# Kernel tuning notes

Measured on AMD Instinct MI355X. Metric: run time of the kernel, lower is better.

## Reference

```python
import jax, jax.numpy as jnp
import numpy as np

SPATIAL_SHAPES = [(128, 128), (64, 64), (32, 32), (16, 16)]  # (H_l, W_l) per level
NUM_HEADS = 8
NUM_LEVELS = 4
NUM_POINTS = 4
EMBED_DIM = 256
HEAD_DIM = EMBED_DIM // NUM_HEADS
LEN_V = sum(h * w for h, w in SPATIAL_SHAPES)  # 21760
BS, LQ = 8, 900


def setup_inputs() -> dict:
    key = jax.random.key(0)
    ks = jax.random.split(key, 12)
    s = 0.05
    return {
        'query': jax.random.normal(ks[0], (BS, LQ, EMBED_DIM), jnp.float32),
        'reference_points': jax.random.uniform(ks[1], (BS, LQ, NUM_LEVELS, 2), jnp.float32),
        'value': jax.random.normal(ks[2], (BS, LEN_V, EMBED_DIM), jnp.float32),
        'w_value': jax.random.normal(ks[3], (EMBED_DIM, EMBED_DIM), jnp.float32) * s,
        'b_value': jnp.zeros((EMBED_DIM,), jnp.float32),
        'w_off': jax.random.normal(ks[4], (EMBED_DIM, NUM_HEADS * NUM_LEVELS * NUM_POINTS * 2), jnp.float32) * s,
        'b_off': jax.random.normal(ks[5], (NUM_HEADS * NUM_LEVELS * NUM_POINTS * 2,), jnp.float32),
        'w_attn': jax.random.normal(ks[6], (EMBED_DIM, NUM_HEADS * NUM_LEVELS * NUM_POINTS), jnp.float32) * s,
        'b_attn': jnp.zeros((NUM_HEADS * NUM_LEVELS * NUM_POINTS,), jnp.float32),
        'w_out': jax.random.normal(ks[7], (EMBED_DIM, EMBED_DIM), jnp.float32) * s,
        'b_out': jnp.zeros((EMBED_DIM,), jnp.float32),
    }


def _bilinear_sample(val, locx, locy, H, W):
    # val: [bs, nh, H*W, hd]; locx/locy: [bs, nh, N] normalized in [0,1]
    # grid_sample semantics: align_corners=False, zero padding.
    px = locx * W - 0.5
    py = locy * H - 0.5
    x0 = jnp.floor(px)
    y0 = jnp.floor(py)
    dx = px - x0
    dy = py - y0
    x0i = x0.astype(jnp.int32)
    y0i = y0.astype(jnp.int32)
    out = jnp.zeros(val.shape[:2] + (locx.shape[-1], val.shape[-1]), val.dtype)
    corners = [
        (x0i, y0i, (1 - dx) * (1 - dy)),
        (x0i + 1, y0i, dx * (1 - dy)),
        (x0i, y0i + 1, (1 - dx) * dy),
        (x0i + 1, y0i + 1, dx * dy),
    ]
    for xi, yi, w in corners:
        valid = ((xi >= 0) & (xi < W) & (yi >= 0) & (yi < H)).astype(val.dtype)
        idx = jnp.clip(yi, 0, H - 1) * W + jnp.clip(xi, 0, W - 1)
        g = jnp.take_along_axis(val, idx[..., None], axis=2)  # [bs,nh,N,hd]
        out = out + g * (w * valid)[..., None]
    return out


def reference(query, reference_points, value, w_value, b_value, w_off, b_off,
              w_attn, b_attn, w_out, b_out):
    bs, Lq, C = query.shape
    # value projection -> [bs, Lv, nh, hd]
    v = (value @ w_value + b_value).reshape(bs, -1, NUM_HEADS, HEAD_DIM)
    # sampling offsets [bs,Lq,nh,L,P,2], attention weights softmax over L*P
    off = (query @ w_off + b_off).reshape(bs, Lq, NUM_HEADS, NUM_LEVELS, NUM_POINTS, 2)
    aw = (query @ w_attn + b_attn).reshape(bs, Lq, NUM_HEADS, NUM_LEVELS * NUM_POINTS)
    aw = jax.nn.softmax(aw, axis=-1).reshape(bs, Lq, NUM_HEADS, NUM_LEVELS, NUM_POINTS)
    # normalizer is (W_l, H_l) per level (flip of spatial shapes)
    norm = jnp.asarray([[w, h] for h, w in SPATIAL_SHAPES], query.dtype)  # [L,2]
    loc = reference_points[:, :, None, :, None, :] + off / norm[None, None, None, :, None, :]
    # per-level bilinear sampling and weighted reduction
    out = jnp.zeros((bs, Lq, NUM_HEADS, HEAD_DIM), query.dtype)
    start = 0
    for l, (H, W) in enumerate(SPATIAL_SHAPES):
        vl = v[:, start:start + H * W]                       # [bs,HW,nh,hd]
        vl = vl.transpose(0, 2, 1, 3)                        # [bs,nh,HW,hd]
        ll = loc[:, :, :, l].transpose(0, 2, 1, 3, 4)        # [bs,nh,Lq,P,2]
        ll = ll.reshape(bs, NUM_HEADS, Lq * NUM_POINTS, 2)
        s = _bilinear_sample(vl, ll[..., 0], ll[..., 1], H, W)
        s = s.reshape(bs, NUM_HEADS, Lq, NUM_POINTS, HEAD_DIM)
        out = out + jnp.einsum('bhqpd,bqhp->bqhd', s, aw[:, :, :, l])
        start += H * W
    out = out.reshape(bs, Lq, C)
    return out @ w_out + b_out
```

## Files before the change

kernel.cpp:

```cpp
#include <hip/hip_runtime.h>

#define BS 8
#define LQ 900
#define NH 8
#define NL 4
#define NP 4
#define HD 32
#define ED 256
#define LEN_V 21760

typedef __attribute__((ext_vector_type(8))) short bf16x8;
typedef __attribute__((ext_vector_type(4))) float f32x4;
typedef __attribute__((ext_vector_type(4))) float fv4;

static __device__ __forceinline__ unsigned short f2bf(float f) {
  union { float f; unsigned u; } x; x.f = f;
  unsigned r = x.u + 0x7fffu + ((x.u >> 16) & 1u);
  return (unsigned short)(r >> 16);
}
static __device__ __forceinline__ float bf_lo(unsigned u) {
  union { unsigned u; float f; } x; x.u = u << 16;
  return x.f;
}
static __device__ __forceinline__ float bf_hi(unsigned u) {
  union { unsigned u; float f; } x; x.u = u & 0xffff0000u;
  return x.f;
}
static __device__ __forceinline__ unsigned pack2(float a, float b) {
  return (unsigned)f2bf(a) | ((unsigned)f2bf(b) << 16);
}

__global__ __launch_bounds__(256) void bprep_kernel(
    const float* __restrict__ w, unsigned short* __restrict__ Bsw) {
  const int id = blockIdx.x * 256 + threadIdx.x;
  const int n = id & 255;
  const int kseg = (id >> 8) & 3;
  const int kc = id >> 10;
  const float* src = &w[(kc * 32 + kseg * 8) * 256 + n];
  float f[8];
#pragma unroll
  for (int j = 0; j < 8; j++) f[j] = src[j * 256];
  uint4 pk;
  pk.x = pack2(f[0], f[1]);
  pk.y = pack2(f[2], f[3]);
  pk.z = pack2(f[4], f[5]);
  pk.w = pack2(f[6], f[7]);
  *(uint4*)&Bsw[((kc * 4 + kseg) * 256 + n) * 8] = pk;
}

__global__ __launch_bounds__(256, 4) void vproj_kernel(
    const float* __restrict__ value, const unsigned short* __restrict__ Bsw,
    const float* __restrict__ bias, unsigned short* __restrict__ vout) {
  const int t = threadIdx.x;
  const int row0 = blockIdx.x * 64;
  const int wv = t >> 6;
  const int lane = t & 63;
  const int quad = lane >> 4;
  const int nn = lane & 15;

  __shared__ unsigned short a_lds[4 * 64 * 8];

  f32x4 acc[4][4];
#pragma unroll
  for (int i = 0; i < 4; i++)
#pragma unroll
    for (int j = 0; j < 4; j++) acc[i][j] = (f32x4)(0.f);

  const int arow = t >> 2;
  const int akseg = t & 3;
  const unsigned short* bptr = &Bsw[(quad * 256 + wv * 64 + nn) * 8];

  for (int kc = 0; kc < 8; kc++) {
    __syncthreads();
    {
      const float* pa = &value[(row0 + arow) * 256 + kc * 32 + akseg * 8];
      fv4 v0 = __builtin_nontemporal_load((const fv4*)pa);
      fv4 v1 = __builtin_nontemporal_load((const fv4*)(pa + 4));
      uint4 pk;
      pk.x = pack2(v0.x, v0.y);
      pk.y = pack2(v0.z, v0.w);
      pk.z = pack2(v1.x, v1.y);
      pk.w = pack2(v1.z, v1.w);
      *(uint4*)&a_lds[(akseg * 64 + arow) * 8] = pk;
    }
    __syncthreads();

    bf16x8 af[4], bfr[4];
#pragma unroll
    for (int ct = 0; ct < 4; ct++)
      bfr[ct] = *(const bf16x8*)(bptr + (kc * 1024 + ct * 16) * 8);
#pragma unroll
    for (int rt = 0; rt < 4; rt++)
      af[rt] = *(const bf16x8*)&a_lds[(quad * 64 + rt * 16 + nn) * 8];
#pragma unroll
    for (int rt = 0; rt < 4; rt++)
#pragma unroll
      for (int ct = 0; ct < 4; ct++)
        acc[rt][ct] = __builtin_amdgcn_mfma_f32_16x16x32_bf16(
            af[rt], bfr[ct], acc[rt][ct], 0, 0, 0);
  }

  const int bb = row0 / LEN_V;
  const int s0 = row0 - bb * LEN_V;
#pragma unroll
  for (int ct = 0; ct < 4; ct++) {
    const int col = wv * 64 + ct * 16 + nn;
    const float bv = bias[col];
    const int h = col >> 5;
    const int d = col & 31;
    unsigned short* vb = &vout[((bb * NH + h) * LEN_V + s0) * HD + d];
#pragma unroll
    for (int rt = 0; rt < 4; rt++) {
      f32x4 f = acc[rt][ct];
#pragma unroll
      for (int reg = 0; reg < 4; reg++) {
        const int s = rt * 16 + quad * 4 + reg;
        vb[s * HD] = f2bf(f[reg] + bv);
      }
    }
  }
}

__global__ __launch_bounds__(384, 2) void offattn_kernel(
    const float* __restrict__ query,
    const float* __restrict__ w_off, const float* __restrict__ b_off,
    const float* __restrict__ w_attn, const float* __restrict__ b_attn,
    float* __restrict__ OFF, float* __restrict__ LOG) {
  const int t = threadIdx.x;
  const int row0 = blockIdx.x * 32;
  const int rg = t / 96;
  const int c4 = t % 96;
  const int col = c4 * 4;
  const bool isOff = col < 256;
  const float* wbase = isOff ? (w_off + col) : (w_attn + (col - 256));
  const int wstride = isOff ? 256 : 128;
  const float* bb = isOff ? (b_off + col) : (b_attn + (col - 256));
  __shared__ float a_lds[32][8];

  float4 acc[8];
#pragma unroll
  for (int r = 0; r < 8; r++) acc[r] = make_float4(0.f, 0.f, 0.f, 0.f);

  for (int k0 = 0; k0 < 256; k0 += 8) {
    __syncthreads();
    if (t < 256) a_lds[t >> 3][t & 7] = query[(row0 + (t >> 3)) * 256 + k0 + (t & 7)];
    __syncthreads();
    float4 wr[8];
#pragma unroll
    for (int k = 0; k < 8; k++)
      wr[k] = *(const float4*)&wbase[(k0 + k) * wstride];
#pragma unroll
    for (int r = 0; r < 8; r++) {
      const float* ar = &a_lds[rg * 8 + r][0];
      float4 a0 = *(const float4*)&ar[0];
      float4 a1 = *(const float4*)&ar[4];
      float4 s = acc[r];
      s.x += a0.x*wr[0].x + a0.y*wr[1].x + a0.z*wr[2].x + a0.w*wr[3].x
           + a1.x*wr[4].x + a1.y*wr[5].x + a1.z*wr[6].x + a1.w*wr[7].x;
      s.y += a0.x*wr[0].y + a0.y*wr[1].y + a0.z*wr[2].y + a0.w*wr[3].y
           + a1.x*wr[4].y + a1.y*wr[5].y + a1.z*wr[6].y + a1.w*wr[7].y;
      s.z += a0.x*wr[0].z + a0.y*wr[1].z + a0.z*wr[2].z + a0.w*wr[3].z
           + a1.x*wr[4].z + a1.y*wr[5].z + a1.z*wr[6].z + a1.w*wr[7].z;
      s.w += a0.x*wr[0].w + a0.y*wr[1].w + a0.z*wr[2].w + a0.w*wr[3].w
           + a1.x*wr[4].w + a1.y*wr[5].w + a1.z*wr[6].w + a1.w*wr[7].w;
      acc[r] = s;
    }
  }

  const float4 bv = *(const float4*)bb;
#pragma unroll
  for (int r = 0; r < 8; r++) {
    const int grow = row0 + rg * 8 + r;
    float4 o = make_float4(acc[r].x + bv.x, acc[r].y + bv.y,
                           acc[r].z + bv.z, acc[r].w + bv.w);
    if (isOff) *(float4*)&OFF[grow * 256 + col] = o;
    else       *(float4*)&LOG[grow * 128 + (col - 256)] = o;
  }
}

__global__ __launch_bounds__(256, 6) void sample_kernel(
    const float* __restrict__ refp, const unsigned short* __restrict__ vp,
    const float* __restrict__ OFF, const float* __restrict__ LOG,
    float* __restrict__ RES) {
  const int t = threadIdx.x;
  const int b = blockIdx.x / (LQ / 4);
  const int q0 = (blockIdx.x % (LQ / 4)) * 4;

  __shared__ float off_lds[4][256];
  __shared__ float aw_lds[4][128];
  __shared__ float ref_lds[4][4][2];
  __shared__ int   soff[512][4];
  __shared__ float swt[512][4];

#pragma unroll
  for (int qi = 0; qi < 4; qi++)
    off_lds[qi][t] = OFF[(b * LQ + q0 + qi) * 256 + t];
  if (t < 128) {
#pragma unroll
    for (int qi = 0; qi < 4; qi++)
      aw_lds[qi][t] = LOG[(b * LQ + q0 + qi) * 128 + t];
  }
  if (t < 32) {
    const int qi = t >> 3, l = (t >> 1) & 3, xy = t & 1;
    ref_lds[qi][l][xy] = refp[((b * LQ + q0 + qi) * NL + l) * 2 + xy];
  }
  __syncthreads();

  if (t < 32) {
    const int qi = t >> 3, h = t & 7;
    float* a = &aw_lds[qi][h * 16];
    float m = a[0];
#pragma unroll
    for (int i = 1; i < 16; i++) m = fmaxf(m, a[i]);
    float e[16];
    float ssum = 0.f;
#pragma unroll
    for (int i = 0; i < 16; i++) { e[i] = __expf(a[i] - m); ssum += e[i]; }
    const float inv = 1.f / ssum;
#pragma unroll
    for (int i = 0; i < 16; i++) a[i] = e[i] * inv;
  }
  __syncthreads();

#pragma unroll
  for (int ss = 0; ss < 2; ss++) {
    const int sid = t + ss * 256;
    const int p = sid & 3, l = (sid >> 2) & 3, h = (sid >> 4) & 7, qi = sid >> 7;
    const int W = 128 >> l;
    const int base = (l == 0) ? 0 : ((l == 1) ? 16384 : ((l == 2) ? 20480 : 21504));
    const float Wf = (float)W;
    const float refx = ref_lds[qi][l][0];
    const float refy = ref_lds[qi][l][1];
    const float offx = off_lds[qi][h * 32 + l * 8 + p * 2 + 0];
    const float offy = off_lds[qi][h * 32 + l * 8 + p * 2 + 1];
    const float aw = aw_lds[qi][h * 16 + l * 4 + p];
    const float px = refx * Wf + offx - 0.5f;
    const float py = refy * Wf + offy - 0.5f;
    const float x0f = floorf(px), y0f = floorf(py);
    const float dx = px - x0f, dy = py - y0f;
    const int x0 = (int)x0f, y0 = (int)y0f;
    const int x1 = x0 + 1, y1 = y0 + 1;
    const float mx0 = (x0 >= 0 && x0 < W) ? 1.f : 0.f;
    const float mx1 = (x1 >= 0 && x1 < W) ? 1.f : 0.f;
    const float my0 = (y0 >= 0 && y0 < W) ? 1.f : 0.f;
    const float my1 = (y1 >= 0 && y1 < W) ? 1.f : 0.f;
    const int x0c = min(max(x0, 0), W - 1);
    const int x1c = min(max(x1, 0), W - 1);
    const int y0c = min(max(y0, 0), W - 1);
    const int y1c = min(max(y1, 0), W - 1);
    soff[sid][0] = (base + y0c * W + x0c) * 8;
    soff[sid][1] = (base + y0c * W + x1c) * 8;
    soff[sid][2] = (base + y1c * W + x0c) * 8;
    soff[sid][3] = (base + y1c * W + x1c) * 8;
    swt[sid][0] = (1.f - dx) * (1.f - dy) * mx0 * my0 * aw;
    swt[sid][1] = dx * (1.f - dy) * mx1 * my0 * aw;
    swt[sid][2] = (1.f - dx) * dy * mx0 * my1 * aw;
    swt[sid][3] = dx * dy * mx1 * my1 * aw;
  }
  __syncthreads();

  const int qi = t >> 6;
  const int hh = (t >> 3) & 7;
  const int d4 = t & 7;
  const uint2* vpu2 = (const uint2*)vp + (size_t)(b * NH + hh) * (LEN_V * HD / 4);
  float r0 = 0.f, r1 = 0.f, r2 = 0.f, r3 = 0.f;
  const int sbase = (qi * 8 + hh) << 4;
#pragma unroll 4
  for (int lp = 0; lp < 16; lp++) {
    const int sid = sbase + lp;
    const int4 o = *(const int4*)&soff[sid][0];
    const float4 w = *(const float4*)&swt[sid][0];
    const uint2 u00 = vpu2[o.x + d4];
    const uint2 u10 = vpu2[o.y + d4];
    const uint2 u01 = vpu2[o.z + d4];
    const uint2 u11 = vpu2[o.w + d4];
    r0 += w.x * bf_lo(u00.x) + w.y * bf_lo(u10.x) + w.z * bf_lo(u01.x) + w.w * bf_lo(u11.x);
    r1 += w.x * bf_hi(u00.x) + w.y * bf_hi(u10.x) + w.z * bf_hi(u01.x) + w.w * bf_hi(u11.x);
    r2 += w.x * bf_lo(u00.y) + w.y * bf_lo(u10.y) + w.z * bf_lo(u01.y) + w.w * bf_lo(u11.y);
    r3 += w.x * bf_hi(u00.y) + w.y * bf_hi(u10.y) + w.z * bf_hi(u01.y) + w.w * bf_hi(u11.y);
  }
  float4 rr = make_float4(r0, r1, r2, r3);
  *(float4*)&RES[(b * LQ + q0 + qi) * 256 + hh * 32 + d4 * 4] = rr;
}

__global__ __launch_bounds__(256, 2) void outproj_kernel(
    const float* __restrict__ RES, const float* __restrict__ w,
    const float* __restrict__ bias, float* __restrict__ out) {
  const int t = threadIdx.x;
  const int row0 = blockIdx.x * 32;
  const int rg = t >> 6;
  const int c0 = (t & 63) << 2;
  __shared__ float a_lds[32][8];

  float4 acc[8];
#pragma unroll
  for (int r = 0; r < 8; r++) acc[r] = make_float4(0.f, 0.f, 0.f, 0.f);

  const int lr = t >> 3;
  const int lk = t & 7;
  for (int k0 = 0; k0 < 256; k0 += 8) {
    __syncthreads();
    a_lds[lr][lk] = RES[(row0 + lr) * 256 + k0 + lk];
    __syncthreads();
    float4 wr[8];
#pragma unroll
    for (int k = 0; k < 8; k++)
      wr[k] = *(const float4*)&w[(k0 + k) * 256 + c0];
#pragma unroll
    for (int r = 0; r < 8; r++) {
      const float* ar = &a_lds[rg * 8 + r][0];
      float4 a0 = *(const float4*)&ar[0];
      float4 a1 = *(const float4*)&ar[4];
      float4 s = acc[r];
      s.x += a0.x*wr[0].x + a0.y*wr[1].x + a0.z*wr[2].x + a0.w*wr[3].x
           + a1.x*wr[4].x + a1.y*wr[5].x + a1.z*wr[6].x + a1.w*wr[7].x;
      s.y += a0.x*wr[0].y + a0.y*wr[1].y + a0.z*wr[2].y + a0.w*wr[3].y
           + a1.x*wr[4].y + a1.y*wr[5].y + a1.z*wr[6].y + a1.w*wr[7].y;
      s.z += a0.x*wr[0].z + a0.y*wr[1].z + a0.z*wr[2].z + a0.w*wr[3].z
           + a1.x*wr[4].z + a1.y*wr[5].z + a1.z*wr[6].z + a1.w*wr[7].z;
      s.w += a0.x*wr[0].w + a0.y*wr[1].w + a0.z*wr[2].w + a0.w*wr[3].w
           + a1.x*wr[4].w + a1.y*wr[5].w + a1.z*wr[6].w + a1.w*wr[7].w;
      acc[r] = s;
    }
  }

  const float4 bv = *(const float4*)&bias[c0];
#pragma unroll
  for (int r = 0; r < 8; r++) {
    const int grow = row0 + rg * 8 + r;
    float4 o = make_float4(acc[r].x + bv.x, acc[r].y + bv.y,
                           acc[r].z + bv.z, acc[r].w + bv.w);
    *(float4*)&out[grow * 256 + c0] = o;
  }
}

extern "C" void kernel_launch(void* const* d_in, const int* in_sizes, int n_in,
                              void* d_out, int out_size, void* d_ws, size_t ws_size,
                              hipStream_t stream) {
  (void)in_sizes; (void)n_in; (void)out_size; (void)ws_size;
  const float* query   = (const float*)d_in[0];
  const float* refp    = (const float*)d_in[1];
  const float* value   = (const float*)d_in[2];
  const float* w_value = (const float*)d_in[3];
  const float* b_value = (const float*)d_in[4];
  const float* w_off   = (const float*)d_in[5];
  const float* b_off   = (const float*)d_in[6];
  const float* w_attn  = (const float*)d_in[7];
  const float* b_attn  = (const float*)d_in[8];
  const float* w_out   = (const float*)d_in[9];
  const float* b_out   = (const float*)d_in[10];
  float* out = (float*)d_out;

  char* ws = (char*)d_ws;
  unsigned short* vp = (unsigned short*)ws;
  float* OFF = (float*)(ws + 89128960);
  float* LOG = (float*)(ws + 89128960 + 7372800);
  float* RES = (float*)(ws + 89128960 + 7372800 + 3686400);
  unsigned short* Bsw = (unsigned short*)(ws + 89128960 + 7372800 + 3686400 + 7372800);

  bprep_kernel<<<32, 256, 0, stream>>>(w_value, Bsw);
  vproj_kernel<<<(BS * LEN_V) / 64, 256, 0, stream>>>(value, Bsw, b_value, vp);
  offattn_kernel<<<(BS * LQ) / 32, 384, 0, stream>>>(query, w_off, b_off,
                                                     w_attn, b_attn, OFF, LOG);
  sample_kernel<<<BS * (LQ / 4), 256, 0, stream>>>(refp, vp, OFF, LOG, RES);
  outproj_kernel<<<(BS * LQ) / 32, 256, 0, stream>>>(RES, w_out, b_out, out);
}
```

Measured before the change: 423.1 us.

## Restructure sampling blocks per (batch, head) with query chunks and XCD-aware mapping

The sample kernel now assigns each block one (batch, head) pair and a chunk of 32 queries, instead of 4 queries across all heads. The block index is remapped so that consecutive work items from the same (batch, head) land on the same XCD (blockIdx & 7 striping). The goal is to improve L2 locality of the head-specific value plane during the bilinear gathers. In exchange, the last chunk has padding work (900 is not a multiple of 32, so the last chunk is partly wasted), and loads of OFF and LOG rows become narrower strided reads.

```diff
diff --git a/kernel.cpp b/kernel.cpp
--- a/kernel.cpp
+++ b/kernel.cpp
@@ -8,6 +8,9 @@
 #define HD 32
 #define ED 256
 #define LEN_V 21760
+
+#define QB 32
+#define QCHUNKS 29
 
 typedef __attribute__((ext_vector_type(8))) short bf16x8;
 typedef __attribute__((ext_vector_type(4))) float f32x4;
@@ -183,32 +186,40 @@
     const float* __restrict__ OFF, const float* __restrict__ LOG,
     float* __restrict__ RES) {
   const int t = threadIdx.x;
-  const int b = blockIdx.x / (LQ / 4);
-  const int q0 = (blockIdx.x % (LQ / 4)) * 4;
-
-  __shared__ float off_lds[4][256];
-  __shared__ float aw_lds[4][128];
-  __shared__ float ref_lds[4][4][2];
-  __shared__ int   soff[512][4];
-  __shared__ float swt[512][4];
-
-#pragma unroll
-  for (int qi = 0; qi < 4; qi++)
-    off_lds[qi][t] = OFF[(b * LQ + q0 + qi) * 256 + t];
-  if (t < 128) {
-#pragma unroll
-    for (int qi = 0; qi < 4; qi++)
-      aw_lds[qi][t] = LOG[(b * LQ + q0 + qi) * 128 + t];
-  }
-  if (t < 32) {
-    const int qi = t >> 3, l = (t >> 1) & 3, xy = t & 1;
-    ref_lds[qi][l][xy] = refp[((b * LQ + q0 + qi) * NL + l) * 2 + xy];
+  const int work = (blockIdx.x & 7) * (8 * QCHUNKS) + (blockIdx.x >> 3);
+  const int pair = work / QCHUNKS;
+  const int qc   = work - pair * QCHUNKS;
+  const int b = pair >> 3;
+  const int h = pair & 7;
+  const int q0 = qc * QB;
+
+  __shared__ float off_lds[QB][32];
+  __shared__ float aw_lds[QB][16];
+  __shared__ float ref_lds[QB][4][2];
+  __shared__ int   soff[QB * 16][4];
+  __shared__ float swt[QB * 16][4];
+
+#pragma unroll
+  for (int rep = 0; rep < 4; rep++) {
+    const int tt = t + rep * 256;
+    const int q = tt >> 5, j = tt & 31;
+    off_lds[q][j] = (q0 + q < LQ) ? OFF[(b * LQ + q0 + q) * 256 + h * 32 + j] : 0.f;
+  }
+#pragma unroll
+  for (int rep = 0; rep < 2; rep++) {
+    const int tt = t + rep * 256;
+    const int q = tt >> 4, j = tt & 15;
+    aw_lds[q][j] = (q0 + q < LQ) ? LOG[(b * LQ + q0 + q) * 128 + h * 16 + j] : 0.f;
+  }
+  {
+    const int q = t >> 3, l = (t >> 1) & 3, xy = t & 1;
+    ref_lds[q][l][xy] = (q0 + q < LQ)
+        ? refp[((b * LQ + q0 + q) * NL + l) * 2 + xy] : 0.5f;
   }
   __syncthreads();
 
-  if (t < 32) {
-    const int qi = t >> 3, h = t & 7;
-    float* a = &aw_lds[qi][h * 16];
+  if (t < QB) {
+    float* a = &aw_lds[t][0];
     float m = a[0];
 #pragma unroll
     for (int i = 1; i < 16; i++) m = fmaxf(m, a[i]);
@@ -225,15 +236,15 @@
 #pragma unroll
   for (int ss = 0; ss < 2; ss++) {
     const int sid = t + ss * 256;
-    const int p = sid & 3, l = (sid >> 2) & 3, h = (sid >> 4) & 7, qi = sid >> 7;
+    const int p = sid & 3, l = (sid >> 2) & 3, q = sid >> 4;
     const int W = 128 >> l;
     const int base = (l == 0) ? 0 : ((l == 1) ? 16384 : ((l == 2) ? 20480 : 21504));
     const float Wf = (float)W;
-    const float refx = ref_lds[qi][l][0];
-    const float refy = ref_lds[qi][l][1];
-    const float offx = off_lds[qi][h * 32 + l * 8 + p * 2 + 0];
-    const float offy = off_lds[qi][h * 32 + l * 8 + p * 2 + 1];
-    const float aw = aw_lds[qi][h * 16 + l * 4 + p];
+    const float refx = ref_lds[q][l][0];
+    const float refy = ref_lds[q][l][1];
+    const float offx = off_lds[q][l * 8 + p * 2 + 0];
+    const float offy = off_lds[q][l * 8 + p * 2 + 1];
+    const float aw = aw_lds[q][l * 4 + p];
     const float px = refx * Wf + offx - 0.5f;
     const float py = refy * Wf + offy - 0.5f;
     const float x0f = floorf(px), y0f = floorf(py);
@@ -259,12 +270,11 @@
   }
   __syncthreads();
 
-  const int qi = t >> 6;
-  const int hh = (t >> 3) & 7;
+  const int q = t >> 3;
   const int d4 = t & 7;
-  const uint2* vpu2 = (const uint2*)vp + (size_t)(b * NH + hh) * (LEN_V * HD / 4);
+  const uint2* vpu2 = (const uint2*)vp + (size_t)(b * NH + h) * (LEN_V * HD / 4);
   float r0 = 0.f, r1 = 0.f, r2 = 0.f, r3 = 0.f;
-  const int sbase = (qi * 8 + hh) << 4;
+  const int sbase = q << 4;
 #pragma unroll 4
   for (int lp = 0; lp < 16; lp++) {
     const int sid = sbase + lp;
@@ -279,8 +289,10 @@
     r2 += w.x * bf_lo(u00.y) + w.y * bf_lo(u10.y) + w.z * bf_lo(u01.y) + w.w * bf_lo(u11.y);
     r3 += w.x * bf_hi(u00.y) + w.y * bf_hi(u10.y) + w.z * bf_hi(u01.y) + w.w * bf_hi(u11.y);
   }
-  float4 rr = make_float4(r0, r1, r2, r3);
-  *(float4*)&RES[(b * LQ + q0 + qi) * 256 + hh * 32 + d4 * 4] = rr;
+  if (q0 + q < LQ) {
+    float4 rr = make_float4(r0, r1, r2, r3);
+    *(float4*)&RES[(b * LQ + q0 + q) * 256 + h * 32 + d4 * 4] = rr;
+  }
 }
 
 __global__ __launch_bounds__(256, 2) void outproj_kernel(
@@ -362,6 +374,6 @@
   vproj_kernel<<<(BS * LEN_V) / 64, 256, 0, stream>>>(value, Bsw, b_value, vp);
   offattn_kernel<<<(BS * LQ) / 32, 384, 0, stream>>>(query, w_off, b_off,
                                                      w_attn, b_attn, OFF, LOG);
-  sample_kernel<<<BS * (LQ / 4), 256, 0, stream>>>(refp, vp, OFF, LOG, RES);
+  sample_kernel<<<64 * QCHUNKS, 256, 0, stream>>>(refp, vp, OFF, LOG, RES);
   outproj_kernel<<<(BS * LQ) / 32, 256, 0, stream>>>(RES, w_out, b_out, out);
 }
```

Result: no change. 417.5 us (-1.3%).

## Fuse offset/attention projection, sampling, and output projection into one kernel

Applied to the files above, without the earlier changes.

Replaces the separate offset/attention GEMM, sampling, and output-projection kernels with one fused kernel that works on 8 queries per block. The intermediates (offsets, logits, sampled results) stay in shared memory instead of going through global buffers. w_out is transposed once in the prep kernel so each thread computes one output column with contiguous weight reads. Each sampling thread now gathers 8 bf16 values per corner instead of 4. The trade-off is that the small projections now run with little data reuse: each block rereads the full weight matrices for only 8 rows, and only 192 of 256 threads do the projection work.

```diff
diff --git a/kernel.cpp b/kernel.cpp
--- a/kernel.cpp
+++ b/kernel.cpp
@@ -9,6 +9,9 @@
 #define ED 256
 #define LEN_V 21760
 
+#define FQ 8
+#define FCHUNKS 113
+
 typedef __attribute__((ext_vector_type(8))) short bf16x8;
 typedef __attribute__((ext_vector_type(4))) float f32x4;
 typedef __attribute__((ext_vector_type(4))) float fv4;
@@ -31,21 +34,33 @@
 }
 
 __global__ __launch_bounds__(256) void bprep_kernel(
-    const float* __restrict__ w, unsigned short* __restrict__ Bsw) {
-  const int id = blockIdx.x * 256 + threadIdx.x;
-  const int n = id & 255;
-  const int kseg = (id >> 8) & 3;
-  const int kc = id >> 10;
-  const float* src = &w[(kc * 32 + kseg * 8) * 256 + n];
-  float f[8];
-#pragma unroll
-  for (int j = 0; j < 8; j++) f[j] = src[j * 256];
-  uint4 pk;
-  pk.x = pack2(f[0], f[1]);
-  pk.y = pack2(f[2], f[3]);
-  pk.z = pack2(f[4], f[5]);
-  pk.w = pack2(f[6], f[7]);
-  *(uint4*)&Bsw[((kc * 4 + kseg) * 256 + n) * 8] = pk;
+    const float* __restrict__ w, unsigned short* __restrict__ Bsw,
+    const float* __restrict__ w_out, float* __restrict__ w_outT) {
+  if (blockIdx.x < 32) {
+    const int id = blockIdx.x * 256 + threadIdx.x;
+    const int n = id & 255;
+    const int kseg = (id >> 8) & 3;
+    const int kc = id >> 10;
+    const float* src = &w[(kc * 32 + kseg * 8) * 256 + n];
+    float f[8];
+#pragma unroll
+    for (int j = 0; j < 8; j++) f[j] = src[j * 256];
+    uint4 pk;
+    pk.x = pack2(f[0], f[1]);
+    pk.y = pack2(f[2], f[3]);
+    pk.z = pack2(f[4], f[5]);
+    pk.w = pack2(f[6], f[7]);
+    *(uint4*)&Bsw[((kc * 4 + kseg) * 256 + n) * 8] = pk;
+  } else {
+    const int id2 = (blockIdx.x - 32) * 256 + threadIdx.x;
+    const int k = id2 >> 6;
+    const int c0 = (id2 & 63) * 4;
+    float4 v = *(const float4*)&w_out[k * 256 + c0];
+    w_outT[(c0 + 0) * 256 + k] = v.x;
+    w_outT[(c0 + 1) * 256 + k] = v.y;
+    w_outT[(c0 + 2) * 256 + k] = v.z;
+    w_outT[(c0 + 3) * 256 + k] = v.w;
+  }
 }
 
 __global__ __launch_bounds__(256, 4) void vproj_kernel(
@@ -121,92 +136,93 @@
   }
 }
 
-__global__ __launch_bounds__(384, 2) void offattn_kernel(
-    const float* __restrict__ query,
+__global__ __launch_bounds__(256, 4) void fused_kernel(
+    const float* __restrict__ query, const float* __restrict__ refp,
+    const unsigned short* __restrict__ vp,
     const float* __restrict__ w_off, const float* __restrict__ b_off,
     const float* __restrict__ w_attn, const float* __restrict__ b_attn,
-    float* __restrict__ OFF, float* __restrict__ LOG) {
+    const float* __restrict__ w_outT, const float* __restrict__ b_out,
+    float* __restrict__ out) {
   const int t = threadIdx.x;
-  const int row0 = blockIdx.x * 32;
-  const int rg = t / 96;
-  const int c4 = t % 96;
-  const int col = c4 * 4;
-  const bool isOff = col < 256;
-  const float* wbase = isOff ? (w_off + col) : (w_attn + (col - 256));
-  const int wstride = isOff ? 256 : 128;
-  const float* bb = isOff ? (b_off + col) : (b_attn + (col - 256));
-  __shared__ float a_lds[32][8];
-
-  float4 acc[8];
-#pragma unroll
-  for (int r = 0; r < 8; r++) acc[r] = make_float4(0.f, 0.f, 0.f, 0.f);
-
-  for (int k0 = 0; k0 < 256; k0 += 8) {
-    __syncthreads();
-    if (t < 256) a_lds[t >> 3][t & 7] = query[(row0 + (t >> 3)) * 256 + k0 + (t & 7)];
-    __syncthreads();
-    float4 wr[8];
-#pragma unroll
-    for (int k = 0; k < 8; k++)
-      wr[k] = *(const float4*)&wbase[(k0 + k) * wstride];
-#pragma unroll
-    for (int r = 0; r < 8; r++) {
-      const float* ar = &a_lds[rg * 8 + r][0];
-      float4 a0 = *(const float4*)&ar[0];
-      float4 a1 = *(const float4*)&ar[4];
-      float4 s = acc[r];
-      s.x += a0.x*wr[0].x + a0.y*wr[1].x + a0.z*wr[2].x + a0.w*wr[3].x
-           + a1.x*wr[4].x + a1.y*wr[5].x + a1.z*wr[6].x + a1.w*wr[7].x;
-      s.y += a0.x*wr[0].y + a0.y*wr[1].y + a0.z*wr[2].y + a0.w*wr[3].y
-           + a1.x*wr[4].y + a1.y*wr[5].y + a1.z*wr[6].y + a1.w*wr[7].y;
-      s.z += a0.x*wr[0].z + a0.y*wr[1].z + a0.z*wr[2].z + a0.w*wr[3].z
-           + a1.x*wr[4].z + a1.y*wr[5].z + a1.z*wr[6].z + a1.w*wr[7].z;
-      s.w += a0.x*wr[0].w + a0.y*wr[1].w + a0.z*wr[2].w + a0.w*wr[3].w
-           + a1.x*wr[4].w + a1.y*wr[5].w + a1.z*wr[6].w + a1.w*wr[7].w;
-      acc[r] = s;
-    }
-  }
-
-  const float4 bv = *(const float4*)bb;
-#pragma unroll
-  for (int r = 0; r < 8; r++) {
-    const int grow = row0 + rg * 8 + r;
-    float4 o = make_float4(acc[r].x + bv.x, acc[r].y + bv.y,
-                           acc[r].z + bv.z, acc[r].w + bv.w);
-    if (isOff) *(float4*)&OFF[grow * 256 + col] = o;
-    else       *(float4*)&LOG[grow * 128 + (col - 256)] = o;
-  }
-}
-
-__global__ __launch_bounds__(256, 6) void sample_kernel(
-    const float* __restrict__ refp, const unsigned short* __restrict__ vp,
-    const float* __restrict__ OFF, const float* __restrict__ LOG,
-    float* __restrict__ RES) {
-  const int t = threadIdx.x;
-  const int b = blockIdx.x / (LQ / 4);
-  const int q0 = (blockIdx.x % (LQ / 4)) * 4;
-
-  __shared__ float off_lds[4][256];
-  __shared__ float aw_lds[4][128];
-  __shared__ float ref_lds[4][4][2];
-  __shared__ int   soff[512][4];
-  __shared__ float swt[512][4];
-
-#pragma unroll
-  for (int qi = 0; qi < 4; qi++)
-    off_lds[qi][t] = OFF[(b * LQ + q0 + qi) * 256 + t];
-  if (t < 128) {
-#pragma unroll
-    for (int qi = 0; qi < 4; qi++)
-      aw_lds[qi][t] = LOG[(b * LQ + q0 + qi) * 128 + t];
-  }
-  if (t < 32) {
+  const int b = blockIdx.x & 7;
+  const int chunk = blockIdx.x >> 3;
+  const int q0 = chunk * FQ;
+
+  __shared__ float q_lds[FQ][256];
+  __shared__ float off_lds[FQ][256];
+  __shared__ float aw_lds[FQ][128];
+  __shared__ float ref_lds[FQ][4][2];
+  __shared__ float res_lds[FQ][256];
+
+  {
+    const int qi = t >> 5;
+    const int j = (t & 31) << 3;
+    if (q0 + qi < LQ) {
+      float4 a = *(const float4*)&query[(b * LQ + q0 + qi) * 256 + j];
+      float4 c = *(const float4*)&query[(b * LQ + q0 + qi) * 256 + j + 4];
+      *(float4*)&q_lds[qi][j] = a;
+      *(float4*)&q_lds[qi][j + 4] = c;
+    } else {
+      *(float4*)&q_lds[qi][j] = make_float4(0.f, 0.f, 0.f, 0.f);
+      *(float4*)&q_lds[qi][j + 4] = make_float4(0.f, 0.f, 0.f, 0.f);
+    }
+  }
+  if (t < 64) {
     const int qi = t >> 3, l = (t >> 1) & 3, xy = t & 1;
-    ref_lds[qi][l][xy] = refp[((b * LQ + q0 + qi) * NL + l) * 2 + xy];
+    ref_lds[qi][l][xy] = (q0 + qi < LQ)
+        ? refp[((b * LQ + q0 + qi) * NL + l) * 2 + xy] : 0.5f;
   }
   __syncthreads();
 
-  if (t < 32) {
+  if (t < 192) {
+    const int rg = t / 96;
+    const int c4 = t % 96;
+    const int col = c4 * 4;
+    const bool isOff = col < 256;
+    const float* wbase = isOff ? (w_off + col) : (w_attn + (col - 256));
+    const int wstride = isOff ? 256 : 128;
+    const float* bb = isOff ? (b_off + col) : (b_attn + (col - 256));
+
+    float4 acc[4];
+#pragma unroll
+    for (int r = 0; r < 4; r++) acc[r] = make_float4(0.f, 0.f, 0.f, 0.f);
+
+    for (int k0 = 0; k0 < 256; k0 += 8) {
+      float4 wr[8];
+#pragma unroll
+      for (int k = 0; k < 8; k++)
+        wr[k] = *(const float4*)&wbase[(k0 + k) * wstride];
+#pragma unroll
+      for (int r = 0; r < 4; r++) {
+        const float* ar = &q_lds[rg * 4 + r][k0];
+        float4 a0 = *(const float4*)&ar[0];
+        float4 a1 = *(const float4*)&ar[4];
+        float4 s = acc[r];
+        s.x += a0.x*wr[0].x + a0.y*wr[1].x + a0.z*wr[2].x + a0.w*wr[3].x
+             + a1.x*wr[4].x + a1.y*wr[5].x + a1.z*wr[6].x + a1.w*wr[7].x;
+        s.y += a0.x*wr[0].y + a0.y*wr[1].y + a0.z*wr[2].y + a0.w*wr[3].y
+             + a1.x*wr[4].y + a1.y*wr[5].y + a1.z*wr[6].y + a1.w*wr[7].y;
+        s.z += a0.x*wr[0].z + a0.y*wr[1].z + a0.z*wr[2].z + a0.w*wr[3].z
+             + a1.x*wr[4].z + a1.y*wr[5].z + a1.z*wr[6].z + a1.w*wr[7].z;
+        s.w += a0.x*wr[0].w + a0.y*wr[1].w + a0.z*wr[2].w + a0.w*wr[3].w
+             + a1.x*wr[4].w + a1.y*wr[5].w + a1.z*wr[6].w + a1.w*wr[7].w;
+        acc[r] = s;
+      }
+    }
+
+    const float4 bv = *(const float4*)bb;
+#pragma unroll
+    for (int r = 0; r < 4; r++) {
+      const int q = rg * 4 + r;
+      float4 o = make_float4(acc[r].x + bv.x, acc[r].y + bv.y,
+                             acc[r].z + bv.z, acc[r].w + bv.w);
+      if (isOff) *(float4*)&off_lds[q][col] = o;
+      else       *(float4*)&aw_lds[q][col - 256] = o;
+    }
+  }
+  __syncthreads();
+
+  if (t < 64) {
     const int qi = t >> 3, h = t & 7;
     float* a = &aw_lds[qi][h * 16];
     float m = a[0];
@@ -222,115 +238,86 @@
   }
   __syncthreads();
 
-#pragma unroll
-  for (int ss = 0; ss < 2; ss++) {
-    const int sid = t + ss * 256;
-    const int p = sid & 3, l = (sid >> 2) & 3, h = (sid >> 4) & 7, qi = sid >> 7;
-    const int W = 128 >> l;
-    const int base = (l == 0) ? 0 : ((l == 1) ? 16384 : ((l == 2) ? 20480 : 21504));
-    const float Wf = (float)W;
-    const float refx = ref_lds[qi][l][0];
-    const float refy = ref_lds[qi][l][1];
-    const float offx = off_lds[qi][h * 32 + l * 8 + p * 2 + 0];
-    const float offy = off_lds[qi][h * 32 + l * 8 + p * 2 + 1];
-    const float aw = aw_lds[qi][h * 16 + l * 4 + p];
-    const float px = refx * Wf + offx - 0.5f;
-    const float py = refy * Wf + offy - 0.5f;
-    const float x0f = floorf(px), y0f = floorf(py);
-    const float dx = px - x0f, dy = py - y0f;
-    const int x0 = (int)x0f, y0 = (int)y0f;
-    const int x1 = x0 + 1, y1 = y0 + 1;
-    const float mx0 = (x0 >= 0 && x0 < W) ? 1.f : 0.f;
-    const float mx1 = (x1 >= 0 && x1 < W) ? 1.f : 0.f;
-    const float my0 = (y0 >= 0 && y0 < W) ? 1.f : 0.f;
-    const float my1 = (y1 >= 0 && y1 < W) ? 1.f : 0.f;
-    const int x0c = min(max(x0, 0), W - 1);
-    const int x1c = min(max(x1, 0), W - 1);
-    const int y0c = min(max(y0, 0), W - 1);
-    const int y1c = min(max(y1, 0), W - 1);
-    soff[sid][0] = (base + y0c * W + x0c) * 8;
-    soff[sid][1] = (base + y0c * W + x1c) * 8;
-    soff[sid][2] = (base + y1c * W + x0c) * 8;
-    soff[sid][3] = (base + y1c * W + x1c) * 8;
-    swt[sid][0] = (1.f - dx) * (1.f - dy) * mx0 * my0 * aw;
-    swt[sid][1] = dx * (1.f - dy) * mx1 * my0 * aw;
-    swt[sid][2] = (1.f - dx) * dy * mx0 * my1 * aw;
-    swt[sid][3] = dx * dy * mx1 * my1 * aw;
+  {
+    const int q = t >> 5;
+    const int h = (t >> 2) & 7;
+    const int d8 = t & 3;
+    const uint4* vpu4 = (const uint4*)vp + (size_t)(b * NH + h) * (LEN_V * HD / 8);
+    float r[8];
+#pragma unroll
+    for (int j = 0; j < 8; j++) r[j] = 0.f;
+
+#pragma unroll
+    for (int l = 0; l < 4; l++) {
+      const int W = 128 >> l;
+      const int base = (l == 0) ? 0 : ((l == 1) ? 16384 : ((l == 2) ? 20480 : 21504));
+      const float Wf = (float)W;
+      const float refx = ref_lds[q][l][0];
+      const float refy = ref_lds[q][l][1];
+#pragma unroll
+      for (int p = 0; p < 4; p++) {
+        const float offx = off_lds[q][h * 32 + l * 8 + p * 2 + 0];
+        const float offy = off_lds[q][h * 32 + l * 8 + p * 2 + 1];
+        const float aw = aw_lds[q][h * 16 + l * 4 + p];
+        const float px = refx * Wf + offx - 0.5f;
+        const float py = refy * Wf + offy - 0.5f;
+        const float x0f = floorf(px), y0f = floorf(py);
+        const float dx = px - x0f, dy = py - y0f;
+        const int x0 = (int)x0f, y0 = (int)y0f;
+        const int x1 = x0 + 1, y1 = y0 + 1;
+        const float mx0 = (x0 >= 0 && x0 < W) ? 1.f : 0.f;
+        const float mx1 = (x1 >= 0 && x1 < W) ? 1.f : 0.f;
+        const float my0 = (y0 >= 0 && y0 < W) ? 1.f : 0.f;
+        const float my1 = (y1 >= 0 && y1 < W) ? 1.f : 0.f;
+        const int x0c = min(max(x0, 0), W - 1);
+        const int x1c = min(max(x1, 0), W - 1);
+        const int y0c = min(max(y0, 0), W - 1);
+        const int y1c = min(max(y1, 0), W - 1);
+        const float w0 = (1.f - dx) * (1.f - dy) * mx0 * my0 * aw;
+        const float w1 = dx * (1.f - dy) * mx1 * my0 * aw;
+        const float w2 = (1.f - dx) * dy * mx0 * my1 * aw;
+        const float w3 = dx * dy * mx1 * my1 * aw;
+        const int o00 = (base + y0c * W + x0c) * 4 + d8;
+        const int o10 = (base + y0c * W + x1c) * 4 + d8;
+        const int o01 = (base + y1c * W + x0c) * 4 + d8;
+        const int o11 = (base + y1c * W + x1c) * 4 + d8;
+        const uint4 u00 = vpu4[o00];
+        const uint4 u10 = vpu4[o10];
+        const uint4 u01 = vpu4[o01];
+        const uint4 u11 = vpu4[o11];
+        r[0] += w0 * bf_lo(u00.x) + w1 * bf_lo(u10.x) + w2 * bf_lo(u01.x) + w3 * bf_lo(u11.x);
+        r[1] += w0 * bf_hi(u00.x) + w1 * bf_hi(u10.x) + w2 * bf_hi(u01.x) + w3 * bf_hi(u11.x);
+        r[2] += w0 * bf_lo(u00.y) + w1 * bf_lo(u10.y) + w2 * bf_lo(u01.y) + w3 * bf_lo(u11.y);
+        r[3] += w0 * bf_hi(u00.y) + w1 * bf_hi(u10.y) + w2 * bf_hi(u01.y) + w3 * bf_hi(u11.y);
+        r[4] += w0 * bf_lo(u00.z) + w1 * bf_lo(u10.z) + w2 * bf_lo(u01.z) + w3 * bf_lo(u11.z);
+        r[5] += w0 * bf_hi(u00.z) + w1 * bf_hi(u10.z) + w2 * bf_hi(u01.z) + w3 * bf_hi(u11.z);
+        r[6] += w0 * bf_lo(u00.w) + w1 * bf_lo(u10.w) + w2 * bf_lo(u01.w) + w3 * bf_lo(u11.w);
+        r[7] += w0 * bf_hi(u00.w) + w1 * bf_hi(u10.w) + w2 * bf_hi(u01.w) + w3 * bf_hi(u11.w);
+      }
+    }
+    *(float4*)&res_lds[q][h * 32 + d8 * 8] = make_float4(r[0], r[1], r[2], r[3]);
+    *(float4*)&res_lds[q][h * 32 + d8 * 8 + 4] = make_float4(r[4], r[5], r[6], r[7]);
   }
   __syncthreads();
 
-  const int qi = t >> 6;
-  const int hh = (t >> 3) & 7;
-  const int d4 = t & 7;
-  const uint2* vpu2 = (const uint2*)vp + (size_t)(b * NH + hh) * (LEN_V * HD / 4);
-  float r0 = 0.f, r1 = 0.f, r2 = 0.f, r3 = 0.f;
-  const int sbase = (qi * 8 + hh) << 4;
-#pragma unroll 4
-  for (int lp = 0; lp < 16; lp++) {
-    const int sid = sbase + lp;
-    const int4 o = *(const int4*)&soff[sid][0];
-    const float4 w = *(const float4*)&swt[sid][0];
-    const uint2 u00 = vpu2[o.x + d4];
-    const uint2 u10 = vpu2[o.y + d4];
-    const uint2 u01 = vpu2[o.z + d4];
-    const uint2 u11 = vpu2[o.w + d4];
-    r0 += w.x * bf_lo(u00.x) + w.y * bf_lo(u10.x) + w.z * bf_lo(u01.x) + w.w * bf_lo(u11.x);
-    r1 += w.x * bf_hi(u00.x) + w.y * bf_hi(u10.x) + w.z * bf_hi(u01.x) + w.w * bf_hi(u11.x);
-    r2 += w.x * bf_lo(u00.y) + w.y * bf_lo(u10.y) + w.z * bf_lo(u01.y) + w.w * bf_lo(u11.y);
-    r3 += w.x * bf_hi(u00.y) + w.y * bf_hi(u10.y) + w.z * bf_hi(u01.y) + w.w * bf_hi(u11.y);
-  }
-  float4 rr = make_float4(r0, r1, r2, r3);
-  *(float4*)&RES[(b * LQ + q0 + qi) * 256 + hh * 32 + d4 * 4] = rr;
-}
-
-__global__ __launch_bounds__(256, 2) void outproj_kernel(
-    const float* __restrict__ RES, const float* __restrict__ w,
-    const float* __restrict__ bias, float* __restrict__ out) {
-  const int t = threadIdx.x;
-  const int row0 = blockIdx.x * 32;
-  const int rg = t >> 6;
-  const int c0 = (t & 63) << 2;
-  __shared__ float a_lds[32][8];
-
-  float4 acc[8];
-#pragma unroll
-  for (int r = 0; r < 8; r++) acc[r] = make_float4(0.f, 0.f, 0.f, 0.f);
-
-  const int lr = t >> 3;
-  const int lk = t & 7;
-  for (int k0 = 0; k0 < 256; k0 += 8) {
-    __syncthreads();
-    a_lds[lr][lk] = RES[(row0 + lr) * 256 + k0 + lk];
-    __syncthreads();
-    float4 wr[8];
-#pragma unroll
-    for (int k = 0; k < 8; k++)
-      wr[k] = *(const float4*)&w[(k0 + k) * 256 + c0];
-#pragma unroll
-    for (int r = 0; r < 8; r++) {
-      const float* ar = &a_lds[rg * 8 + r][0];
-      float4 a0 = *(const float4*)&ar[0];
-      float4 a1 = *(const float4*)&ar[4];
-      float4 s = acc[r];
-      s.x += a0.x*wr[0].x + a0.y*wr[1].x + a0.z*wr[2].x + a0.w*wr[3].x
-           + a1.x*wr[4].x + a1.y*wr[5].x + a1.z*wr[6].x + a1.w*wr[7].x;
-      s.y += a0.x*wr[0].y + a0.y*wr[1].y + a0.z*wr[2].y + a0.w*wr[3].y
-           + a1.x*wr[4].y + a1.y*wr[5].y + a1.z*wr[6].y + a1.w*wr[7].y;
-      s.z += a0.x*wr[0].z + a0.y*wr[1].z + a0.z*wr[2].z + a0.w*wr[3].z
-           + a1.x*wr[4].z + a1.y*wr[5].z + a1.z*wr[6].z + a1.w*wr[7].z;
-      s.w += a0.x*wr[0].w + a0.y*wr[1].w + a0.z*wr[2].w + a0.w*wr[3].w
-           + a1.x*wr[4].w + a1.y*wr[5].w + a1.z*wr[6].w + a1.w*wr[7].w;
-      acc[r] = s;
-    }
-  }
-
-  const float4 bv = *(const float4*)&bias[c0];
-#pragma unroll
-  for (int r = 0; r < 8; r++) {
-    const int grow = row0 + rg * 8 + r;
-    float4 o = make_float4(acc[r].x + bv.x, acc[r].y + bv.y,
-                           acc[r].z + bv.z, acc[r].w + bv.w);
-    *(float4*)&out[grow * 256 + c0] = o;
+  {
+    float r8[8];
+#pragma unroll
+    for (int q = 0; q < 8; q++) r8[q] = 0.f;
+    const float* wt = &w_outT[t * 256];
+    for (int k = 0; k < 256; k += 4) {
+      float4 wv = *(const float4*)&wt[k];
+#pragma unroll
+      for (int q = 0; q < 8; q++) {
+        r8[q] += wv.x * res_lds[q][k] + wv.y * res_lds[q][k + 1]
+               + wv.z * res_lds[q][k + 2] + wv.w * res_lds[q][k + 3];
+      }
+    }
+    const float bo = b_out[t];
+#pragma unroll
+    for (int q = 0; q < 8; q++) {
+      if (q0 + q < LQ) out[(b * LQ + q0 + q) * 256 + t] = r8[q] + bo;
+    }
   }
 }
 
@@ -352,16 +339,13 @@
   float* out = (float*)d_out;
 
   char* ws = (char*)d_ws;
-  unsigned short* vp = (unsigned short*)ws;
-  float* OFF = (float*)(ws + 89128960);
-  float* LOG = (float*)(ws + 89128960 + 7372800);
-  float* RES = (float*)(ws + 89128960 + 7372800 + 3686400);
-  unsigned short* Bsw = (unsigned short*)(ws + 89128960 + 7372800 + 3686400 + 7372800);
-
-  bprep_kernel<<<32, 256, 0, stream>>>(w_value, Bsw);
+  unsigned short* vp  = (unsigned short*)ws;
+  unsigned short* Bsw = (unsigned short*)(ws + 89128960);
+  float* w_outT       = (float*)(ws + 89128960 + 131072);
+
+  bprep_kernel<<<96, 256, 0, stream>>>(w_value, Bsw, w_out, w_outT);
   vproj_kernel<<<(BS * LEN_V) / 64, 256, 0, stream>>>(value, Bsw, b_value, vp);
-  offattn_kernel<<<(BS * LQ) / 32, 384, 0, stream>>>(query, w_off, b_off,
-                                                     w_attn, b_attn, OFF, LOG);
-  sample_kernel<<<BS * (LQ / 4), 256, 0, stream>>>(refp, vp, OFF, LOG, RES);
-  outproj_kernel<<<(BS * LQ) / 32, 256, 0, stream>>>(RES, w_out, b_out, out);
-}
+  fused_kernel<<<BS * FCHUNKS, 256, 0, stream>>>(query, refp, vp,
+                                                 w_off, b_off, w_attn, b_attn,
+                                                 w_outT, b_out, out);
+}
```

After: 504.0 us. 1.19x slower.
